# Kernel optimization log

Measured on AMD Instinct MI355X. Metric: run time of the kernel, lower is better.

## Reference

```python
import jax, jax.numpy as jnp
import numpy as np

B, G, D, L, NH = 4, 30, 320, 4, 8
DK = D // NH
S = G * G
FF = 4 * D
EPS = 1e-5

FLOAT_KEYS = ['pe', 'in_emb_w', 'in_emb_b', 'wq', 'bq', 'wk', 'bk', 'wv', 'bv', 'wo', 'bo',
              'ln_a_g', 'ln_a_b', 'dist_emb', 'dir_emb', 'w_rot', 'b_rot', 'w_refl', 'b_refl',
              'w_tr', 'b_tr', 'w_sc', 'b_sc', 'tn_w1', 'tn_b1', 'tn_w2', 'tn_b2', 'tn_w3', 'tn_b3',
              'ff_w1', 'ff_b1', 'ff_w2', 'ff_b2', 'ln2_g', 'ln2_b', 'ck1', 'cb1', 'ck3', 'cb3',
              'ck5', 'cb5', 'ck7', 'cb7', 'fus_w', 'fus_b', 'op_w1', 'op_b1', 'op_w2', 'op_b2',
              'op_w3', 'op_b3']


def _make_pe():
    # Faithful vectorization of GeometricPositionalEncoding's triple loop.
    pe = np.zeros((G, G, D), dtype=np.float32)
    i = np.arange(0, D // 2, 2)                       # 0,2,...,158
    div = 10000.0 ** (i / D)
    h = np.arange(G, dtype=np.float64)
    sh = np.sin(h[:, None] / div)[:, None, :]
    ch = np.cos(h[:, None] / div)[:, None, :]
    pe[:, :, i] = sh
    pe[:, :, i + 1] = ch
    sw = np.sin(h[:, None] / div)[None, :, :]
    cw = np.cos(h[:, None] / div)[None, :, :]
    pe[:, :, i + D // 2] = sw
    pe[:, :, i + D // 2 + 1] = cw
    hh, ww = np.meshgrid(np.arange(G), np.arange(G), indexing='ij')
    c = G // 2
    pe[:, :, -4] = np.sqrt((hh - c) ** 2 + (ww - c) ** 2) / G   # overwrites last 4 dims, as in torch
    pe[:, :, -3] = hh / G
    pe[:, :, -2] = ww / G
    pe[:, :, -1] = (hh + ww) / (2 * G)
    return pe


def _make_geo_indices():
    # Precompute _compute_geometric_bias index tables (distance bin, direction octant).
    idx = np.arange(S)
    hc, wc = idx // G, idx % G
    dh = hc[None, :] - hc[:, None]                    # h2 - h1 at [i, j]
    dw = wc[None, :] - wc[:, None]
    dist = np.minimum(np.sqrt(dh ** 2 + dw ** 2).astype(np.int32), 59)
    ang = np.arctan2(dh.astype(np.float64), dw.astype(np.float64))
    dirn = ((ang + np.pi) / (2 * np.pi / 8)).astype(np.int32) % 8
    dirn[(dh == 0) & (dw == 0)] = 0
    return dist.astype(np.int32), dirn.astype(np.int32)


def _ln(x, g, b):
    m = x.mean(-1, keepdims=True)
    v = ((x - m) ** 2).mean(-1, keepdims=True)
    return (x - m) * jax.lax.rsqrt(v + EPS) * g + b


def _gelu(x):
    return jax.nn.gelu(x, approximate=False)  # torch nn.GELU default (erf)


def _forward(p, input_grid, dist_idx, dir_idx):
    x = jax.nn.one_hot(input_grid[:, 0], 10, dtype=jnp.float32)   # [B,G,G,10]
    x = x @ p['in_emb_w'] + p['in_emb_b']                          # [B,G,G,D]
    x = x + p['pe'][None]
    scale = 1.0 / np.sqrt(DK)
    for l in range(L):
        xs = x.reshape(B, S, D)
        def heads(w, b):
            return (xs @ w + b).reshape(B, S, NH, DK).transpose(0, 2, 1, 3)
        q = heads(p['wq'][l], p['bq'][l])
        k = heads(p['wk'][l], p['bk'][l])
        v = heads(p['wv'][l], p['bv'][l])
        # geometric bias via embedding gathers: [S,S,NH] -> [NH,S,S]
        bias = p['dist_emb'][l][dist_idx] + p['dir_emb'][l][dir_idx]
        scores = jnp.einsum('bhsd,bhtd->bhst', q, k) * scale + bias.transpose(2, 0, 1)[None]
        attn = jax.nn.softmax(scores, axis=-1)
        out = jnp.einsum('bhst,bhtd->bhsd', attn, v).transpose(0, 2, 1, 3).reshape(B, S, D)
        xs = _ln(out @ p['wo'][l] + p['bo'][l] + xs, p['ln_a_g'][l], p['ln_a_b'][l])
        # geometric transformation module
        g = xs.mean(1)                                              # [B,D] global mean over H,W
        tp = jnp.concatenate([
            jax.nn.softmax(g @ p['w_rot'][l] + p['b_rot'][l], axis=-1),
            jax.nn.softmax(g @ p['w_refl'][l] + p['b_refl'][l], axis=-1),
            jnp.tanh(g @ p['w_tr'][l] + p['b_tr'][l]),
            jax.nn.softmax(g @ p['w_sc'][l] + p['b_sc'][l], axis=-1)], axis=-1)   # [B,17]
        ti = jnp.concatenate([xs, jnp.broadcast_to(tp[:, None, :], (B, S, 17))], axis=-1)
        t = _gelu(ti @ p['tn_w1'][l] + p['tn_b1'][l])
        t = _gelu(t @ p['tn_w2'][l] + p['tn_b2'][l])
        t = t @ p['tn_w3'][l] + p['tn_b3'][l]
        xs = xs + 0.3 * t
        # feed-forward with post-LN residual
        f = _gelu(xs @ p['ff_w1'][l] + p['ff_b1'][l]) @ p['ff_w2'][l] + p['ff_b2'][l]
        xs = _ln(f + xs, p['ln2_g'][l], p['ln2_b'][l])
        x = xs.reshape(B, G, G, D)
    # multiscale conv fusion (NHWC, SAME padding == torch padding=k//2 for odd k)
    dn = ('NHWC', 'HWIO', 'NHWC')
    feats = [jax.nn.relu(jax.lax.conv_general_dilated(x, p['ck%d' % kk], (1, 1), 'SAME',
                                                      dimension_numbers=dn) + p['cb%d' % kk])
             for kk in (1, 3, 5, 7)]
    fused = jnp.concatenate(feats, axis=-1) @ p['fus_w'] + p['fus_b']
    h1 = _gelu(fused @ p['op_w1'] + p['op_b1'])
    h2 = _gelu(h1 @ p['op_w2'] + p['op_b2'])
    return h2 @ p['op_w3'] + p['op_b3']                            # [B,G,G,10] logits


def setup_inputs():
    key = jax.random.key(0)
    ks = iter(jax.random.split(key, 80))
    w = lambda *s: (0.02 * jax.random.normal(next(ks), s)).astype(jnp.float32)
    z = lambda *s: jnp.zeros(s, jnp.float32)
    inp = dict(
        input_grid=jax.random.randint(next(ks), (B, 1, G, G), 0, 10, dtype=jnp.int32),
        pe=jnp.asarray(_make_pe()),
        in_emb_w=w(10, D), in_emb_b=z(D),
        wq=w(L, D, D), bq=z(L, D), wk=w(L, D, D), bk=z(L, D),
        wv=w(L, D, D), bv=z(L, D), wo=w(L, D, D), bo=z(L, D),
        ln_a_g=jnp.ones((L, D), jnp.float32), ln_a_b=z(L, D),
        dist_emb=w(L, 60, NH), dir_emb=w(L, 8, NH),
        w_rot=w(L, D, 4), b_rot=z(L, 4), w_refl=w(L, D, 8), b_refl=z(L, 8),
        w_tr=w(L, D, 2), b_tr=z(L, 2), w_sc=w(L, D, 3), b_sc=z(L, 3),
        tn_w1=w(L, D + 17, 2 * D), tn_b1=z(L, 2 * D),
        tn_w2=w(L, 2 * D, D), tn_b2=z(L, D),
        tn_w3=w(L, D, D), tn_b3=z(L, D),
        ff_w1=w(L, D, FF), ff_b1=z(L, FF), ff_w2=w(L, FF, D), ff_b2=z(L, D),
        ln2_g=jnp.ones((L, D), jnp.float32), ln2_b=z(L, D),
        ck1=w(1, 1, D, D), cb1=z(D), ck3=w(3, 3, D, D), cb3=z(D),
        ck5=w(5, 5, D, D), cb5=z(D), ck7=w(7, 7, D, D), cb7=z(D),
        fus_w=w(4 * D, D), fus_b=z(D),
        op_w1=w(D, D // 2), op_b1=z(D // 2),
        op_w2=w(D // 2, D // 4), op_b2=z(D // 4),
        op_w3=w(D // 4, 10), op_b3=z(10),
    )
    di, dr = _make_geo_indices()
    inp['dist_idx'] = jnp.asarray(di)
    inp['dir_idx'] = jnp.asarray(dr)
    return inp


def reference(input_grid, dist_idx, dir_idx, pe, in_emb_w, in_emb_b, wq, bq, wk, bk, wv, bv, wo, bo,
              ln_a_g, ln_a_b, dist_emb, dir_emb, w_rot, b_rot, w_refl, b_refl, w_tr, b_tr, w_sc, b_sc,
              tn_w1, tn_b1, tn_w2, tn_b2, tn_w3, tn_b3, ff_w1, ff_b1, ff_w2, ff_b2, ln2_g, ln2_b,
              ck1, cb1, ck3, cb3, ck5, cb5, ck7, cb7, fus_w, fus_b,
              op_w1, op_b1, op_w2, op_b2, op_w3, op_b3):
    p = dict(zip(FLOAT_KEYS, (pe, in_emb_w, in_emb_b, wq, bq, wk, bk, wv, bv, wo, bo,
                              ln_a_g, ln_a_b, dist_emb, dir_emb, w_rot, b_rot, w_refl, b_refl,
                              w_tr, b_tr, w_sc, b_sc, tn_w1, tn_b1, tn_w2, tn_b2, tn_w3, tn_b3,
                              ff_w1, ff_b1, ff_w2, ff_b2, ln2_g, ln2_b, ck1, cb1, ck3, cb3,
                              ck5, cb5, ck7, cb7, fus_w, fus_b, op_w1, op_b1, op_w2, op_b2,
                              op_w3, op_b3)))
    return _forward(p, input_grid, dist_idx, dir_idx)
```

## Files before the change

### kernel.cpp

```cpp
#include <hip/hip_runtime.h>
#include <hip/hip_bf16.h>

#define BB 4
#define GG_ 30
#define DD 320
#define LL 4
#define NHH 8
#define DKK 40
#define SS 900
#define BS 3600
#define FFD 1280
#define LDK 72

typedef __attribute__((ext_vector_type(8))) short short8;
typedef __attribute__((ext_vector_type(4))) short short4v;
typedef __attribute__((ext_vector_type(4))) float f32x4;

__device__ __forceinline__ float gelu_f(float x) {
    return 0.5f * x * (1.0f + erff(x * 0.70710678118654752f));
}

__device__ __forceinline__ float bfbits2f(short b) {
    return __uint_as_float(((unsigned)(unsigned short)b) << 16);
}

__device__ __forceinline__ void convt_tile(const float* __restrict__ s,
                                           __hip_bfloat16* __restrict__ d,
                                           int K, int N, int Kpad, int kb, int nb) {
    __shared__ float t[32][33];
    const int tx = threadIdx.x, ty = threadIdx.y;
#pragma unroll
    for (int i = 0; i < 4; ++i) {
        int k = kb + ty + i * 8, n = nb + tx;
        t[ty + i * 8][tx] = (k < K && n < N) ? s[(size_t)k * N + n] : 0.f;
    }
    __syncthreads();
#pragma unroll
    for (int i = 0; i < 4; ++i) {
        int n = nb + ty + i * 8, k = kb + tx;
        if (n < N && k < Kpad) d[(size_t)n * Kpad + k] = __float2bfloat16(t[tx][ty + i * 8]);
    }
}

__global__ __launch_bounds__(256) void allconvt_kernel(
    const float* wo, const float* tnw1, const float* tnw2, const float* tnw3,
    const float* ffw1, const float* ffw2, const float* ck1, const float* ck3,
    const float* ck5, const float* ck7, const float* fusw, const float* opw1,
    __hip_bfloat16* WOT, __hip_bfloat16* TN1T, __hip_bfloat16* TN2T, __hip_bfloat16* TN3T,
    __hip_bfloat16* FF1T, __hip_bfloat16* FF2T, __hip_bfloat16* CK1T, __hip_bfloat16* CK3T,
    __hip_bfloat16* CK5T, __hip_bfloat16* CK7T, __hip_bfloat16* FUST, __hip_bfloat16* OP1T) {
    const int bid = blockIdx.x;
    const float* s; __hip_bfloat16* d;
    int K, N, Kpad, gx, per, local, sS, dS;
    if (bid < 400)        { local = bid;         s = wo;   d = WOT;  K = 320;  N = 320;  Kpad = 320;  sS = 102400; dS = 102400; gx = 10;  per = 100; }
    else if (bid < 1360)  { local = bid - 400;   s = tnw1; d = TN1T; K = 337;  N = 640;  Kpad = 384;  sS = 215680; dS = 245760; gx = 12;  per = 240; }
    else if (bid < 2160)  { local = bid - 1360;  s = tnw2; d = TN2T; K = 640;  N = 320;  Kpad = 640;  sS = 204800; dS = 204800; gx = 20;  per = 200; }
    else if (bid < 2560)  { local = bid - 2160;  s = tnw3; d = TN3T; K = 320;  N = 320;  Kpad = 320;  sS = 102400; dS = 102400; gx = 10;  per = 100; }
    else if (bid < 4160)  { local = bid - 2560;  s = ffw1; d = FF1T; K = 320;  N = 1280; Kpad = 320;  sS = 409600; dS = 409600; gx = 10;  per = 400; }
    else if (bid < 5760)  { local = bid - 4160;  s = ffw2; d = FF2T; K = 1280; N = 320;  Kpad = 1280; sS = 409600; dS = 409600; gx = 40;  per = 400; }
    else if (bid < 5860)  { local = bid - 5760;  s = ck1;  d = CK1T; K = 320;  N = 320;  Kpad = 320;  sS = 0; dS = 0; gx = 10;  per = 100; }
    else if (bid < 6760)  { local = bid - 5860;  s = ck3;  d = CK3T; K = 2880; N = 320;  Kpad = 2880; sS = 0; dS = 0; gx = 90;  per = 900; }
    else if (bid < 9260)  { local = bid - 6760;  s = ck5;  d = CK5T; K = 8000; N = 320;  Kpad = 8000; sS = 0; dS = 0; gx = 250; per = 2500; }
    else if (bid < 14160) { local = bid - 9260;  s = ck7;  d = CK7T; K = 15680; N = 320; Kpad = 15680; sS = 0; dS = 0; gx = 490; per = 4900; }
    else if (bid < 14560) { local = bid - 14160; s = fusw; d = FUST; K = 1280; N = 320;  Kpad = 1280; sS = 0; dS = 0; gx = 40;  per = 400; }
    else                  { local = bid - 14560; s = opw1; d = OP1T; K = 320;  N = 160;  Kpad = 320;  sS = 0; dS = 0; gx = 10;  per = 50; }
    const int mat = local / per, rem = local - mat * per;
    const int kb = (rem % gx) * 32, nb = (rem / gx) * 32;
    convt_tile(s + (size_t)mat * sS, d + (size_t)mat * dS, K, N, Kpad, kb, nb);
}

__global__ __launch_bounds__(256) void qkvconvt_kernel(const float* __restrict__ wq,
                                                       const float* __restrict__ wk,
                                                       const float* __restrict__ wv,
                                                       __hip_bfloat16* __restrict__ dst) {
    __shared__ float t[32][33];
    const int z = blockIdx.z, l = z / 3, wsel = z % 3;
    const float* s = (wsel == 0 ? wq : wsel == 1 ? wk : wv) + (size_t)l * 102400;
    __hip_bfloat16* d = dst + (size_t)l * 307200 + wsel * 102400;
    const int kb = blockIdx.x * 32, nb = blockIdx.y * 32;
    const int tx = threadIdx.x, ty = threadIdx.y;
#pragma unroll
    for (int i = 0; i < 4; ++i) {
        int k = kb + ty + i * 8, n = nb + tx;
        t[ty + i * 8][tx] = s[(size_t)k * 320 + n];
    }
    __syncthreads();
#pragma unroll
    for (int i = 0; i < 4; ++i) {
        int n = nb + ty + i * 8, k = kb + tx;
        d[(size_t)n * 320 + k] = __float2bfloat16(t[tx][ty + i * 8]);
    }
}

__global__ void embed_kernel(const int* __restrict__ grid, const float* __restrict__ pe,
                             const float* __restrict__ ew, const float* __restrict__ eb,
                             float* __restrict__ x, __hip_bfloat16* __restrict__ xb) {
    int idx = blockIdx.x * 256 + threadIdx.x;
    int m = idx / DD, d = idx % DD;
    int gv = grid[m];
    float v = ew[gv * DD + d] + eb[d] + pe[(m % SS) * DD + d];
    x[idx] = v;
    xb[idx] = __float2bfloat16(v);
}

__global__ __launch_bounds__(256) void mgemm_kernel(
    const __hip_bfloat16* __restrict__ A, int lda,
    const __hip_bfloat16* __restrict__ Aaux,
    const __hip_bfloat16* __restrict__ Wt, int ldw,
    const float* __restrict__ bias, const float* __restrict__ biasB, const float* __restrict__ biasC,
    const float* __restrict__ res, int ldr,
    float alpha, float* __restrict__ Cf, float* __restrict__ Cf2,
    __hip_bfloat16* __restrict__ Cb, int ldc,
    int M, int N, int K, int act) {
    __shared__ short As[128 * LDK];
    __shared__ short Bs[64 * LDK];
    const int tid = threadIdx.x;
    const int m0 = blockIdx.y * 128, n0 = blockIdx.x * 64;
    const int kb0 = blockIdx.z * K;
    float* __restrict__ CfO = (blockIdx.z == 0) ? Cf : Cf2;
    const int lane = tid & 63;
    const int w = tid >> 6, wm = w >> 1, wn = w & 1;
    const int rbase = tid >> 3, q8 = (tid & 7) * 8;
    f32x4 acc[4][2];
    const f32x4 fz = {0.f, 0.f, 0.f, 0.f};
#pragma unroll
    for (int mi = 0; mi < 4; ++mi)
#pragma unroll
        for (int ni = 0; ni < 2; ++ni) acc[mi][ni] = fz;
    const short8 zz = {0, 0, 0, 0, 0, 0, 0, 0};
    for (int k0 = 0; k0 < K; k0 += 64) {
        const int gk = kb0 + k0;
        const bool auxChunk = (Aaux != nullptr) && (gk == 320);
#pragma unroll
        for (int c = 0; c < 4; ++c) {
            int r = c * 32 + rbase, m = m0 + r;
            short8 v = zz;
            if (m < M) {
                if (auxChunk) {
                    int bidx = m / SS;
#pragma unroll
                    for (int e = 0; e < 8; ++e) {
                        int j = q8 + e;
                        v[e] = (j < 17) ? ((const short*)Aaux)[bidx * 17 + j] : (short)0;
                    }
                } else {
                    v = *(const short8*)((const short*)A + (size_t)m * lda + gk + q8);
                }
            }
            *(short8*)(As + r * LDK + q8) = v;
        }
#pragma unroll
        for (int c = 0; c < 2; ++c) {
            int r = c * 32 + rbase, n = n0 + r;
            short8 v = zz;
            if (n < N) v = *(const short8*)((const short*)Wt + (size_t)n * ldw + gk + q8);
            *(short8*)(Bs + r * LDK + q8) = v;
        }
        __syncthreads();
#pragma unroll
        for (int ks = 0; ks < 64; ks += 32) {
            const int kb = ks + (lane >> 4) * 8;
            short8 af[4], bf[2];
#pragma unroll
            for (int mi = 0; mi < 4; ++mi)
                af[mi] = *(const short8*)(As + (wm * 64 + mi * 16 + (lane & 15)) * LDK + kb);
#pragma unroll
            for (int ni = 0; ni < 2; ++ni)
                bf[ni] = *(const short8*)(Bs + (wn * 32 + ni * 16 + (lane & 15)) * LDK + kb);
#pragma unroll
            for (int mi = 0; mi < 4; ++mi)
#pragma unroll
                for (int ni = 0; ni < 2; ++ni)
                    acc[mi][ni] = __builtin_amdgcn_mfma_f32_16x16x32_bf16(af[mi], bf[ni], acc[mi][ni], 0, 0, 0);
        }
        __syncthreads();
    }
    const int col0 = n0 + wn * 32 + (lane & 15);
    const int rloc = (lane >> 4) * 4;
#pragma unroll
    for (int mi = 0; mi < 4; ++mi) {
#pragma unroll
        for (int ni = 0; ni < 2; ++ni) {
            int col = col0 + ni * 16;
            if (col >= N) continue;
            float bv;
            if (biasC) bv = (col < 320) ? bias[col] : (col < 640) ? biasB[col - 320] : biasC[col - 640];
            else bv = bias ? bias[col] : 0.f;
#pragma unroll
            for (int r = 0; r < 4; ++r) {
                int row = m0 + wm * 64 + mi * 16 + rloc + r;
                if (row >= M) continue;
                float v = acc[mi][ni][r] + bv;
                if (act == 1) v = gelu_f(v);
                else if (act == 2) v = fmaxf(v, 0.f);
                v *= alpha;
                if (res) v += res[(size_t)row * ldr + col];
                if (CfO) CfO[(size_t)row * ldc + col] = v;
                if (Cb) Cb[(size_t)row * ldc + col] = __float2bfloat16(v);
            }
        }
    }
}

__global__ __launch_bounds__(256) void mconvall_kernel(
    const __hip_bfloat16* __restrict__ P, const __hip_bfloat16* __restrict__ W3,
    const __hip_bfloat16* __restrict__ W5, const __hip_bfloat16* __restrict__ W7,
    __hip_bfloat16* __restrict__ part) {
    const int nwg = 1160;
    const int ib = blockIdx.x;
    const int xcd = ib & 7, kk2 = ib >> 3;
    const int qq = nwg >> 3, rr = nwg & 7;
    const int wid = (xcd < rr) ? (xcd * (qq + 1) + kk2) : (rr * (qq + 1) + (xcd - rr) * qq + kk2);
    const int seg = wid / 145, local = wid - seg * 145;
    int KS, t0, t1;
    const __hip_bfloat16* Wt;
    if (seg == 0)      { KS = 3; Wt = W3; t0 = 0; t1 = 9; }
    else if (seg == 1) { KS = 5; Wt = W5; t0 = 0; t1 = 13; }
    else if (seg == 2) { KS = 5; Wt = W5; t0 = 13; t1 = 25; }
    else               { KS = 7; Wt = W7; int z = seg - 3; t0 = z * 10; t1 = (z < 4) ? t0 + 10 : 49; }
    const int slice = seg;
    const int K = KS * KS * DD;
    const int OFF = 3 - KS / 2;
    const int mt = local % 29, nt = local / 29;
    __hip_bfloat16* __restrict__ Cp = part + (size_t)slice * BS * DD;
    __shared__ short As[128 * LDK];
    __shared__ short Bs[64 * LDK];
    const int tid = threadIdx.x;
    const int m0 = mt * 128, n0 = nt * 64;
    const int lane = tid & 63;
    const int w = tid >> 6, wm = w >> 1, wn = w & 1;
    const int rbase = tid >> 3, q8 = (tid & 7) * 8;
    f32x4 acc[4][2];
    const f32x4 fz = {0.f, 0.f, 0.f, 0.f};
#pragma unroll
    for (int mi = 0; mi < 4; ++mi)
#pragma unroll
        for (int ni = 0; ni < 2; ++ni) acc[mi][ni] = fz;
    const short8 zz = {0, 0, 0, 0, 0, 0, 0, 0};
    const short* P0[4];
    bool mval[4];
#pragma unroll
    for (int c = 0; c < 4; ++c) {
        int m = m0 + c * 32 + rbase;
        mval[c] = (m < BS);
        int mm = mval[c] ? m : 0;
        int b = mm / SS, hw = mm % SS, oh = hw / GG_, ow = hw % GG_;
        P0[c] = (const short*)P + (size_t)((b * 36 + oh) * 36 + ow) * DD + q8;
    }
    const short* W0[2];
#pragma unroll
    for (int c = 0; c < 2; ++c) {
        int n = n0 + c * 32 + rbase;
        W0[c] = (const short*)Wt + (size_t)n * K + q8;
    }
    for (int tap = t0; tap < t1; ++tap) {
        const int khr = tap / KS, kw = tap - khr * KS;
        const int tapOff = ((khr + OFF) * 36 + (kw + OFF)) * DD;
        const int wOff = tap * DD;
        for (int ci0 = 0; ci0 < DD; ci0 += 64) {
#pragma unroll
            for (int c = 0; c < 4; ++c) {
                int r = c * 32 + rbase;
                short8 v = mval[c] ? *(const short8*)(P0[c] + tapOff + ci0) : zz;
                *(short8*)(As + r * LDK + q8) = v;
            }
#pragma unroll
            for (int c = 0; c < 2; ++c) {
                int r = c * 32 + rbase;
                short8 v = *(const short8*)(W0[c] + wOff + ci0);
                *(short8*)(Bs + r * LDK + q8) = v;
            }
            __syncthreads();
#pragma unroll
            for (int ks = 0; ks < 64; ks += 32) {
                const int kb = ks + (lane >> 4) * 8;
                short8 af[4], bf[2];
#pragma unroll
                for (int mi = 0; mi < 4; ++mi)
                    af[mi] = *(const short8*)(As + (wm * 64 + mi * 16 + (lane & 15)) * LDK + kb);
#pragma unroll
                for (int ni = 0; ni < 2; ++ni)
                    bf[ni] = *(const short8*)(Bs + (wn * 32 + ni * 16 + (lane & 15)) * LDK + kb);
#pragma unroll
                for (int mi = 0; mi < 4; ++mi)
#pragma unroll
                    for (int ni = 0; ni < 2; ++ni)
                        acc[mi][ni] = __builtin_amdgcn_mfma_f32_16x16x32_bf16(af[mi], bf[ni], acc[mi][ni], 0, 0, 0);
            }
            __syncthreads();
        }
    }
    const int col0 = n0 + wn * 32 + (lane & 15);
    const int rloc = (lane >> 4) * 4;
#pragma unroll
    for (int mi = 0; mi < 4; ++mi) {
#pragma unroll
        for (int ni = 0; ni < 2; ++ni) {
            int col = col0 + ni * 16;
#pragma unroll
            for (int r = 0; r < 4; ++r) {
                int row = m0 + wm * 64 + mi * 16 + rloc + r;
                if (row < BS) Cp[(size_t)row * DD + col] = __float2bfloat16(acc[mi][ni][r]);
            }
        }
    }
}

__global__ __launch_bounds__(256) void creduceall_kernel(const __hip_bfloat16* __restrict__ part,
                                                         const float* __restrict__ cb3,
                                                         const float* __restrict__ cb5,
                                                         const float* __restrict__ cb7,
                                                         __hip_bfloat16* __restrict__ feats) {
    const int PER = BS * DD / 8;
    int idx = blockIdx.x * 256 + threadIdx.x;
    int which = idx / PER;
    if (which >= 3) return;
    int sub = idx - which * PER;
    int row = sub / (DD / 8), c8 = (sub % (DD / 8)) * 8;
    const __hip_bfloat16* basep;
    const float* bias;
    int nsplit, colOff;
    if (which == 0)      { basep = part;                          nsplit = 1; bias = cb3; colOff = 320; }
    else if (which == 1) { basep = part + (size_t)1 * BS * DD;    nsplit = 2; bias = cb5; colOff = 640; }
    else                 { basep = part + (size_t)3 * BS * DD;    nsplit = 5; bias = cb7; colOff = 960; }
    float s[8] = {};
    for (int p = 0; p < nsplit; ++p) {
        short8 v = *(const short8*)((const short*)basep + (size_t)p * BS * DD + (size_t)row * DD + c8);
#pragma unroll
        for (int j = 0; j < 8; ++j) s[j] += bfbits2f(v[j]);
    }
    __hip_bfloat16* o = feats + (size_t)row * 1280 + colOff + c8;
#pragma unroll
    for (int j = 0; j < 8; ++j) o[j] = __float2bfloat16(fmaxf(s[j] + bias[c8 + j], 0.f));
}

__global__ void pad_kernel(const __hip_bfloat16* __restrict__ xb, __hip_bfloat16* __restrict__ p) {
    int idx = blockIdx.x * 256 + threadIdx.x;
    if (idx >= BB * 36 * 36 * DD) return;
    int c = idx % DD, t = idx / DD;
    int wp = t % 36, t2 = t / 36, hp = t2 % 36, b = t2 / 36;
    __hip_bfloat16 v = __float2bfloat16(0.f);
    if (hp >= 3 && hp < 33 && wp >= 3 && wp < 33)
        v = xb[((b * SS + (hp - 3) * GG_ + (wp - 3))) * DD + c];
    p[idx] = v;
}

__global__ __launch_bounds__(256) void gemm_kernel(
    const float* __restrict__ A, int lda, const float* __restrict__ W,
    const float* __restrict__ bias, float* __restrict__ C, int ldc,
    int M, int N, int K, int act) {
    __shared__ float As[16][65];
    __shared__ float Ws[16][65];
    const int tid = threadIdx.x;
    const int m0 = blockIdx.y * 64, n0 = blockIdx.x * 64;
    const int tx = tid & 15, ty = tid >> 4;
    float acc[4][4] = {};
    const int kkA = tid & 15, mloc0 = tid >> 4;
    const int nloc = tid & 63, kk0 = tid >> 6;
    for (int k0 = 0; k0 < K; k0 += 16) {
        const int kA = k0 + kkA;
#pragma unroll
        for (int i = 0; i < 4; ++i) {
            int mloc = mloc0 + i * 16, m = m0 + mloc;
            As[kkA][mloc] = (m < M && kA < K) ? A[m * lda + kA] : 0.f;
        }
#pragma unroll
        for (int i = 0; i < 4; ++i) {
            int kk = kk0 + i * 4, k = k0 + kk, n = n0 + nloc;
            Ws[kk][nloc] = (k < K && n < N) ? W[k * N + n] : 0.f;
        }
        __syncthreads();
#pragma unroll
        for (int kk = 0; kk < 16; ++kk) {
            float a[4], b[4];
#pragma unroll
            for (int i = 0; i < 4; ++i) a[i] = As[kk][ty * 4 + i];
#pragma unroll
            for (int j = 0; j < 4; ++j) b[j] = Ws[kk][tx * 4 + j];
#pragma unroll
            for (int i = 0; i < 4; ++i)
#pragma unroll
                for (int j = 0; j < 4; ++j) acc[i][j] = fmaf(a[i], b[j], acc[i][j]);
        }
        __syncthreads();
    }
#pragma unroll
    for (int i = 0; i < 4; ++i) {
        int m = m0 + ty * 4 + i;
        if (m >= M) continue;
#pragma unroll
        for (int j = 0; j < 4; ++j) {
            int n = n0 + tx * 4 + j;
            if (n >= N) continue;
            float v = acc[i][j] + bias[n];
            if (act == 1) v = gelu_f(v);
            C[m * ldc + n] = v;
        }
    }
}

__global__ __launch_bounds__(256) void attprep_kernel(const float* __restrict__ de,
                                                      const float* __restrict__ dre,
                                                      const int* __restrict__ dist,
                                                      const int* __restrict__ dirn,
                                                      const __hip_bfloat16* __restrict__ QKV,
                                                      __hip_bfloat16* __restrict__ biasOut,
                                                      __hip_bfloat16* __restrict__ VT) {
    const int gid = blockIdx.x;
    const int tid = threadIdx.x;
    if (gid < 3375) {
        int idx = gid * 256 + tid;
        int sq = idx / 960, t = idx - sq * 960;
        float lut[NHH];
        if (t < SS) {
            int dv = dist[sq * SS + t], rv = dirn[sq * SS + t];
#pragma unroll
            for (int h = 0; h < NHH; ++h) lut[h] = de[dv * NHH + h] + dre[rv * NHH + h];
        } else {
#pragma unroll
            for (int h = 0; h < NHH; ++h) lut[h] = 0.f;
        }
#pragma unroll
        for (int h = 0; h < NHH; ++h)
            biasOut[((size_t)h * SS + sq) * 960 + t] = __float2bfloat16(lut[h]);
    } else {
        int vidx = (gid - 3375) * 256 + tid;
        int t0 = (vidx % 240) * 4;
        int d = (vidx / 240) % 48;
        int h = (vidx / (240 * 48)) % NHH;
        int b = vidx / (240 * 48 * NHH);
        short4v v = {0, 0, 0, 0};
        if (d < DKK) {
#pragma unroll
            for (int j = 0; j < 4; ++j) {
                int t = t0 + j;
                if (t < SS)
                    v[j] = ((const short*)QKV)[((size_t)b * SS + t) * 960 + 640 + h * DKK + d];
            }
        }
        *(short4v*)((short*)VT + (((size_t)b * NHH + h) * 48 + d) * 960 + t0) = v;
    }
}

#define LQ 72
#define LK 72
#define LV 72
#define LP 72
__global__ __launch_bounds__(512) void mattn_kernel(
    const __hip_bfloat16* __restrict__ Qg, const __hip_bfloat16* __restrict__ Kg,
    const __hip_bfloat16* __restrict__ VTg, const __hip_bfloat16* __restrict__ BIASg,
    __hip_bfloat16* __restrict__ AO) {
    const int qt = blockIdx.x, h = blockIdx.y, b = blockIdx.z;
    const int tid = threadIdx.x, lane = tid & 63, w = tid >> 6;
    const int wq = w & 3, ws = w >> 2;
    const int tid2 = tid & 255;
    const int lhi = lane >> 4, llo = lane & 15;
    __shared__ short Qs[64 * LQ];
    __shared__ short Ks[2][64 * LK];
    __shared__ short Vs[2][48 * LV];
    __shared__ short Ps[8][16 * LP];
    __shared__ float Lm[4][16];
    __shared__ float Ll[4][16];
    __shared__ float Lo[4][16][DKK];
    short* Ps_w = Ps[w];
    short* Ks_s = Ks[ws];
    short* Vs_s = Vs[ws];
    const int q0 = qt * 64;
    const short4v z4 = {0, 0, 0, 0};
    const f32x4 fz = {0.f, 0.f, 0.f, 0.f};
    const float scale = 0.15811388300841898f;

    for (int task = tid; task < 64 * 16; task += 512) {
        int r = task >> 4, d0 = (task & 15) * 4;
        int q = q0 + r;
        short4v v = z4;
        if (q < SS && d0 < DKK)
            v = *(const short4v*)((const short*)Qg + ((size_t)b * SS + q) * 960 + h * DKK + d0);
        *(short4v*)(Qs + r * LQ + d0) = v;
    }
    __syncthreads();
    short8 qa[2];
#pragma unroll
    for (int ks = 0; ks < 2; ++ks)
        qa[ks] = *(const short8*)(Qs + (wq * 16 + llo) * LQ + ks * 32 + lhi * 8);

    float mrow[4] = {-1e30f, -1e30f, -1e30f, -1e30f};
    float lrow[4] = {0.f, 0.f, 0.f, 0.f};
    f32x4 o[3] = {fz, fz, fz};
    const int qrow = q0 + wq * 16 + lhi * 4;

    for (int tt = 0; tt < 8; ++tt) {
        const int t = tt * 2 + ws;
        const int kv0 = t * 64;
        if (t < 15) {
            for (int task = tid2; task < 64 * 16; task += 256) {
                int r = task >> 4, d0 = (task & 15) * 4;
                int kv = kv0 + r;
                short4v v = z4;
                if (kv < SS && d0 < DKK)
                    v = *(const short4v*)((const short*)Kg + ((size_t)b * SS + kv) * 960 + h * DKK + d0);
                *(short4v*)(Ks_s + r * LK + d0) = v;
            }
            for (int task = tid2; task < 48 * 16; task += 256) {
                int r = task >> 4, c4 = (task & 15) * 4;
                short4v v = *(const short4v*)((const short*)VTg +
                             (((size_t)b * NHH + h) * 48 + r) * 960 + kv0 + c4);
                *(short4v*)(Vs_s + r * LV + c4) = v;
            }
        }
        __syncthreads();
        if (t < 15) {
            f32x4 s[4] = {fz, fz, fz, fz};
#pragma unroll
            for (int ks = 0; ks < 2; ++ks) {
#pragma unroll
                for (int ni = 0; ni < 4; ++ni) {
                    short8 kb = *(const short8*)(Ks_s + (ni * 16 + llo) * LK + ks * 32 + lhi * 8);
                    s[ni] = __builtin_amdgcn_mfma_f32_16x16x32_bf16(qa[ks], kb, s[ni], 0, 0, 0);
                }
            }
#pragma unroll
            for (int ni = 0; ni < 4; ++ni) {
                int col = kv0 + ni * 16 + llo;
#pragma unroll
                for (int r = 0; r < 4; ++r) {
                    int qc = qrow + r; if (qc > SS - 1) qc = SS - 1;
                    float v = s[ni][r] * scale +
                              __bfloat162float(BIASg[((size_t)h * SS + qc) * 960 + col]);
                    s[ni][r] = (col < SS) ? v : -1e30f;
                }
            }
            float rmax[4], psum[4], corr[4];
#pragma unroll
            for (int r = 0; r < 4; ++r)
                rmax[r] = fmaxf(fmaxf(s[0][r], s[1][r]), fmaxf(s[2][r], s[3][r]));
#pragma unroll
            for (int off = 1; off < 16; off <<= 1)
#pragma unroll
                for (int r = 0; r < 4; ++r)
                    rmax[r] = fmaxf(rmax[r], __shfl_xor(rmax[r], off));
#pragma unroll
            for (int r = 0; r < 4; ++r) {
                float mnew = fmaxf(mrow[r], rmax[r]);
                corr[r] = __expf(mrow[r] - mnew);
                mrow[r] = mnew;
                float ps = 0.f;
#pragma unroll
                for (int ni = 0; ni < 4; ++ni) {
                    float p = __expf(s[ni][r] - mnew);
                    s[ni][r] = p;
                    ps += p;
                }
                psum[r] = ps;
            }
#pragma unroll
            for (int off = 1; off < 16; off <<= 1)
#pragma unroll
                for (int r = 0; r < 4; ++r) psum[r] += __shfl_xor(psum[r], off);
#pragma unroll
            for (int r = 0; r < 4; ++r) lrow[r] = lrow[r] * corr[r] + psum[r];
#pragma unroll
            for (int nj = 0; nj < 3; ++nj)
#pragma unroll
                for (int r = 0; r < 4; ++r) o[nj][r] *= corr[r];
#pragma unroll
            for (int ni = 0; ni < 4; ++ni)
#pragma unroll
                for (int r = 0; r < 4; ++r)
                    ((__hip_bfloat16*)Ps_w)[(lhi * 4 + r) * LP + ni * 16 + llo] =
                        __float2bfloat16(s[ni][r]);
#pragma unroll
            for (int ks = 0; ks < 2; ++ks) {
                short8 pa = *(const short8*)(Ps_w + llo * LP + ks * 32 + lhi * 8);
#pragma unroll
                for (int nj = 0; nj < 3; ++nj) {
                    short8 vb = *(const short8*)(Vs_s + (nj * 16 + llo) * LV + ks * 32 + lhi * 8);
                    o[nj] = __builtin_amdgcn_mfma_f32_16x16x32_bf16(pa, vb, o[nj], 0, 0, 0);
                }
            }
        }
        __syncthreads();
    }
    if (ws == 1) {
#pragma unroll
        for (int r = 0; r < 4; ++r) {
            int lr = lhi * 4 + r;
            if (llo == 0) { Lm[wq][lr] = mrow[r]; Ll[wq][lr] = lrow[r]; }
#pragma unroll
            for (int nj = 0; nj < 3; ++nj) {
                int d = nj * 16 + llo;
                if (d < DKK) Lo[wq][lr][d] = o[nj][r];
            }
        }
    }
    __syncthreads();
    if (ws == 0) {
#pragma unroll
        for (int r = 0; r < 4; ++r) {
            int lr = lhi * 4 + r;
            float m1 = Lm[wq][lr], l1 = Ll[wq][lr];
            float m = fmaxf(mrow[r], m1);
            float a0 = __expf(mrow[r] - m), a1 = __expf(m1 - m);
            float linv = 1.f / (lrow[r] * a0 + l1 * a1);
            int q = qrow + r;
            if (q < SS) {
#pragma unroll
                for (int nj = 0; nj < 3; ++nj) {
                    int d = nj * 16 + llo;
                    if (d < DKK)
                        AO[((size_t)b * SS + q) * DD + h * DKK + d] =
                            __float2bfloat16((o[nj][r] * a0 + Lo[wq][lr][d] * a1) * linv);
                }
            }
        }
    }
}

__global__ __launch_bounds__(320) void ln_kernel(const float* __restrict__ a,
                                                 const float* __restrict__ a2,
                                                 const float* __restrict__ cb,
                                                 const float* __restrict__ add,
                                                 const float* __restrict__ g,
                                                 const float* __restrict__ bta,
                                                 float* __restrict__ out,
                                                 __hip_bfloat16* __restrict__ outb) {
    const int row = blockIdx.x, i = threadIdx.x;
    __shared__ float red[320];
    __shared__ float s_m, s_v;
    float v = a[row * DD + i];
    if (a2) v += a2[row * DD + i];
    if (cb) v += cb[i];
    if (add) v += add[row * DD + i];
    red[i] = v;
    __syncthreads();
    if (i < 64) red[i] += red[i + 256];
    __syncthreads();
    for (int s = 128; s > 0; s >>= 1) {
        if (i < s) red[i] += red[i + s];
        __syncthreads();
    }
    if (i == 0) s_m = red[0] * (1.0f / DD);
    __syncthreads();
    const float d = v - s_m;
    red[i] = d * d;
    __syncthreads();
    if (i < 64) red[i] += red[i + 256];
    __syncthreads();
    for (int s = 128; s > 0; s >>= 1) {
        if (i < s) red[i] += red[i + s];
        __syncthreads();
    }
    if (i == 0) s_v = red[0] * (1.0f / DD);
    __syncthreads();
    float o = d * rsqrtf(s_v + 1e-5f) * g[i] + bta[i];
    out[row * DD + i] = o;
    outb[row * DD + i] = __float2bfloat16(o);
}

__global__ __launch_bounds__(256) void mpart_kernel(const float* __restrict__ xs,
                                                    float* __restrict__ mp) {
    const int b = blockIdx.y, z = blockIdx.z;
    const int d = blockIdx.x * 64 + (threadIdx.x & 63);
    const int rg = threadIdx.x >> 6;
    float s = 0.f;
    const int t0 = z * 150;
    for (int t = t0 + rg; t < t0 + 150; t += 4) s += xs[((size_t)b * SS + t) * DD + d];
    __shared__ float red[256];
    red[threadIdx.x] = s;
    __syncthreads();
    if (threadIdx.x < 128) red[threadIdx.x] += red[threadIdx.x + 128];
    __syncthreads();
    if (threadIdx.x < 64) mp[((size_t)b * 6 + z) * DD + d] = red[threadIdx.x] + red[threadIdx.x + 64];
}

__global__ __launch_bounds__(64) void tp_kernel(const float* __restrict__ mp,
                                                const float* __restrict__ wrot, const float* __restrict__ brot,
                                                const float* __restrict__ wrefl, const float* __restrict__ brefl,
                                                const float* __restrict__ wtr, const float* __restrict__ btr,
                                                const float* __restrict__ wsc, const float* __restrict__ bsc,
                                                __hip_bfloat16* __restrict__ tpb) {
    const int b = blockIdx.x, tid = threadIdx.x;
    __shared__ float gs[DD];
    __shared__ float raw[17];
    for (int j = tid; j < DD; j += 64) {
        float s6 = 0.f;
#pragma unroll
        for (int z = 0; z < 6; ++z) s6 += mp[((size_t)b * 6 + z) * DD + j];
        gs[j] = s6 * (1.0f / SS);
    }
    __syncthreads();
    if (tid < 17) {
        float s;
        if (tid < 4) {
            s = brot[tid];
            for (int d = 0; d < DD; ++d) s = fmaf(gs[d], wrot[d * 4 + tid], s);
        } else if (tid < 12) {
            int j = tid - 4;
            s = brefl[j];
            for (int d = 0; d < DD; ++d) s = fmaf(gs[d], wrefl[d * 8 + j], s);
        } else if (tid < 14) {
            int j = tid - 12;
            s = btr[j];
            for (int d = 0; d < DD; ++d) s = fmaf(gs[d], wtr[d * 2 + j], s);
        } else {
            int j = tid - 14;
            s = bsc[j];
            for (int d = 0; d < DD; ++d) s = fmaf(gs[d], wsc[d * 3 + j], s);
        }
        raw[tid] = s;
    }
    __syncthreads();
    if (tid == 0) {
        float mx = -1e30f;
        for (int j = 0; j < 4; ++j) mx = fmaxf(mx, raw[j]);
        float sm = 0.f, e[4];
        for (int j = 0; j < 4; ++j) { e[j] = expf(raw[j] - mx); sm += e[j]; }
        for (int j = 0; j < 4; ++j) tpb[b * 17 + j] = __float2bfloat16(e[j] / sm);
    } else if (tid == 1) {
        float mx = -1e30f;
        for (int j = 4; j < 12; ++j) mx = fmaxf(mx, raw[j]);
        float sm = 0.f, e[8];
        for (int j = 0; j < 8; ++j) { e[j] = expf(raw[4 + j] - mx); sm += e[j]; }
        for (int j = 0; j < 8; ++j) tpb[b * 17 + 4 + j] = __float2bfloat16(e[j] / sm);
    } else if (tid == 2) {
        tpb[b * 17 + 12] = __float2bfloat16(tanhf(raw[12]));
        tpb[b * 17 + 13] = __float2bfloat16(tanhf(raw[13]));
    } else if (tid == 3) {
        float mx = -1e30f;
        for (int j = 14; j < 17; ++j) mx = fmaxf(mx, raw[j]);
        float sm = 0.f, e[3];
        for (int j = 0; j < 3; ++j) { e[j] = expf(raw[14 + j] - mx); sm += e[j]; }
        for (int j = 0; j < 3; ++j) tpb[b * 17 + 14 + j] = __float2bfloat16(e[j] / sm);
    }
}

static inline void launch_mgemm(hipStream_t s, const __hip_bfloat16* A, int lda,
                                const __hip_bfloat16* Aaux,
                                const __hip_bfloat16* Wt, int ldw, const float* bias,
                                const float* biasB, const float* biasC,
                                const float* res, int ldr, float alpha, float* Cf,
                                __hip_bfloat16* Cb, int ldc, int M, int N, int K, int act) {
    dim3 g((N + 63) / 64, (M + 127) / 128);
    mgemm_kernel<<<g, 256, 0, s>>>(A, lda, Aaux, Wt, ldw, bias, biasB, biasC, res, ldr, alpha,
                                   Cf, nullptr, Cb, ldc, M, N, K, act);
}

extern "C" void kernel_launch(void* const* d_in, const int* in_sizes, int n_in,
                              void* d_out, int out_size, void* d_ws, size_t ws_size,
                              hipStream_t stream) {
    (void)in_sizes; (void)n_in; (void)out_size; (void)ws_size;
    const int* in_grid = (const int*)d_in[0];
    const float* pe = (const float*)d_in[1];
    const float* iew = (const float*)d_in[2];
    const float* ieb = (const float*)d_in[3];
    const float* wq = (const float*)d_in[4], *bq = (const float*)d_in[5];
    const float* wk = (const float*)d_in[6], *bk = (const float*)d_in[7];
    const float* wv = (const float*)d_in[8], *bv = (const float*)d_in[9];
    const float* wo = (const float*)d_in[10], *bo = (const float*)d_in[11];
    const float* lnag = (const float*)d_in[12], *lnab = (const float*)d_in[13];
    const float* dist_emb = (const float*)d_in[14], *dir_emb = (const float*)d_in[15];
    const float* wrot = (const float*)d_in[16], *brot = (const float*)d_in[17];
    const float* wrefl = (const float*)d_in[18], *brefl = (const float*)d_in[19];
    const float* wtr = (const float*)d_in[20], *btr = (const float*)d_in[21];
    const float* wsc = (const float*)d_in[22], *bsc = (const float*)d_in[23];
    const float* tnw1 = (const float*)d_in[24], *tnb1 = (const float*)d_in[25];
    const float* tnw2 = (const float*)d_in[26], *tnb2 = (const float*)d_in[27];
    const float* tnw3 = (const float*)d_in[28], *tnb3 = (const float*)d_in[29];
    const float* ffw1 = (const float*)d_in[30], *ffb1 = (const float*)d_in[31];
    const float* ffw2 = (const float*)d_in[32], *ffb2 = (const float*)d_in[33];
    const float* ln2g = (const float*)d_in[34], *ln2b = (const float*)d_in[35];
    const float* ck1 = (const float*)d_in[36], *cb1 = (const float*)d_in[37];
    const float* ck3 = (const float*)d_in[38], *cb3 = (const float*)d_in[39];
    const float* ck5 = (const float*)d_in[40], *cb5 = (const float*)d_in[41];
    const float* ck7 = (const float*)d_in[42], *cb7 = (const float*)d_in[43];
    const float* fusw = (const float*)d_in[44], *fusb = (const float*)d_in[45];
    const float* opw1 = (const float*)d_in[46], *opb1 = (const float*)d_in[47];
    const float* opw2 = (const float*)d_in[48], *opb2 = (const float*)d_in[49];
    const float* opw3 = (const float*)d_in[50], *opb3 = (const float*)d_in[51];
    const int* dist_idx = (const int*)d_in[52];
    const int* dir_idx = (const int*)d_in[53];
    float* out = (float*)d_out;

    char* base = (char*)d_ws;
    typedef __hip_bfloat16 bf;
    bf* WQKVT = (bf*)(base + 0);
    bf* WOT = (bf*)(base + 2457600);
    bf* TN1T = (bf*)(base + 3276800);
    bf* TN2T = (bf*)(base + 5242880);
    bf* TN3T = (bf*)(base + 6881280);
    bf* FF1T = (bf*)(base + 7700480);
    bf* FF2T = (bf*)(base + 10977280);
    bf* CK1T = (bf*)(base + 14254080);
    bf* CK3T = (bf*)(base + 14458880);
    bf* CK5T = (bf*)(base + 16302080);
    bf* CK7T = (bf*)(base + 21422080);
    bf* FUST = (bf*)(base + 31457280);
    bf* OP1T = (bf*)(base + 32276480);
    float* XS = (float*)(base + 32378880);
    bf* XSbf = (bf*)(base + 36986880);
    bf* QKVbf = (bf*)(base + 39290880);
    bf* VT = (bf*)(base + 46202880);
    float* P1f = (float*)(base + 39290880);
    float* R2 = (float*)(base + 53114880);
    bf* TPbf = (bf*)(base + 57728000);
    bf* CPART = (bf*)(base + 39290880);
    char* BIG = base + 57728512;
    bf* AObf = (bf*)(BIG + 0);
    float* MPart = (float*)(BIG + 0);
    bf* BIAS = (bf*)(BIG + 2764800);
    bf* T1bf = (bf*)(BIG + 2764800);
    bf* T2bf = (bf*)(BIG + 7372800);
    bf* F1bf = (bf*)(BIG + 0);
    bf* PADbf = (bf*)(BIG + 0);
    bf* FEATSbf = (bf*)(BIG + 3317760);
    float* H1 = (float*)(BIG + 0);
    float* H2 = (float*)(BIG + 2304000);
    bf* R2bf = XSbf;

    dim3 cb(32, 8);
    qkvconvt_kernel<<<dim3(10, 10, 12), cb, 0, stream>>>(wq, wk, wv, WQKVT);
    allconvt_kernel<<<14610, cb, 0, stream>>>(wo, tnw1, tnw2, tnw3, ffw1, ffw2,
                                              ck1, ck3, ck5, ck7, fusw, opw1,
                                              WOT, TN1T, TN2T, TN3T, FF1T, FF2T,
                                              CK1T, CK3T, CK5T, CK7T, FUST, OP1T);

    embed_kernel<<<4500, 256, 0, stream>>>(in_grid, pe, iew, ieb, XS, XSbf);

    for (int l = 0; l < LL; ++l) {
        const int wO = l * DD * DD, bO = l * DD;
        launch_mgemm(stream, XSbf, DD, nullptr, WQKVT + l * 307200, 320, bq + bO, bk + bO, bv + bO,
                     nullptr, 0, 1.f, nullptr, QKVbf, 960, BS, 960, 320, 0);
        attprep_kernel<<<4815, 256, 0, stream>>>(dist_emb + l * 60 * NHH, dir_emb + l * 8 * NHH,
                                                 dist_idx, dir_idx, QKVbf, BIAS, VT);
        mattn_kernel<<<dim3(15, NHH, BB), 512, 0, stream>>>(QKVbf, QKVbf + 320, VT, BIAS, AObf);
        launch_mgemm(stream, AObf, DD, nullptr, WOT + wO, DD, bo + bO, nullptr, nullptr, XS, DD, 1.f,
                     R2, nullptr, DD, BS, DD, DD, 0);
        ln_kernel<<<BS, 320, 0, stream>>>(R2, nullptr, nullptr, nullptr, lnag + bO, lnab + bO, XS, XSbf);
        mpart_kernel<<<dim3(5, BB, 6), 256, 0, stream>>>(XS, MPart);
        tp_kernel<<<BB, 64, 0, stream>>>(MPart, wrot + l * 1280, brot + l * 4,
                                         wrefl + l * 2560, brefl + l * 8,
                                         wtr + l * 640, btr + l * 2,
                                         wsc + l * 960, bsc + l * 3, TPbf);
        launch_mgemm(stream, XSbf, DD, TPbf, TN1T + l * 245760, 384, tnb1 + l * 640, nullptr,
                     nullptr, nullptr, 0, 1.f, nullptr, T1bf, 640, BS, 640, 384, 1);
        launch_mgemm(stream, T1bf, 640, nullptr, TN2T + l * 204800, 640, tnb2 + bO, nullptr,
                     nullptr, nullptr, 0, 1.f, nullptr, T2bf, DD, BS, DD, 640, 1);
        launch_mgemm(stream, T2bf, DD, nullptr, TN3T + wO, DD, tnb3 + bO, nullptr, nullptr, XS, DD,
                     0.3f, XS, XSbf, DD, BS, DD, DD, 0);
        launch_mgemm(stream, XSbf, DD, nullptr, FF1T + l * 409600, DD, ffb1 + l * FFD, nullptr,
                     nullptr, nullptr, 0, 1.f, nullptr, F1bf, FFD, BS, FFD, DD, 1);
        {
            dim3 g(5, 29, 2);
            mgemm_kernel<<<g, 256, 0, stream>>>(F1bf, FFD, nullptr, FF2T + l * 409600, FFD,
                                                nullptr, nullptr, nullptr, nullptr, 0, 1.f,
                                                R2, P1f, nullptr, DD, BS, DD, 640, 0);
        }
        ln_kernel<<<BS, 320, 0, stream>>>(R2, P1f, ffb2 + bO, XS, ln2g + bO, ln2b + bO, XS, XSbf);
    }

    pad_kernel<<<(BB * 36 * 36 * DD + 255) / 256, 256, 0, stream>>>(XSbf, PADbf);
    launch_mgemm(stream, XSbf, DD, nullptr, CK1T, DD, cb1, nullptr, nullptr, nullptr, 0, 1.f,
                 nullptr, FEATSbf + 0, 1280, BS, DD, DD, 2);
    mconvall_kernel<<<1160, 256, 0, stream>>>(PADbf, CK3T, CK5T, CK7T, CPART);
    creduceall_kernel<<<(3 * BS * DD / 8 + 255) / 256, 256, 0, stream>>>(CPART, cb3, cb5, cb7, FEATSbf);
    launch_mgemm(stream, FEATSbf, 1280, nullptr, FUST, 1280, fusb, nullptr, nullptr, nullptr, 0, 1.f,
                 nullptr, R2bf, DD, BS, DD, 1280, 0);
    launch_mgemm(stream, R2bf, DD, nullptr, OP1T, DD, opb1, nullptr, nullptr, nullptr, 0, 1.f,
                 H1, nullptr, 160, BS, 160, DD, 1);
    gemm_kernel<<<dim3(2, 57), 256, 0, stream>>>(H1, 160, opw2, opb2, H2, 80, BS, 80, 160, 1);
    gemm_kernel<<<dim3(1, 57), 256, 0, stream>>>(H2, 80, opw3, opb3, out, 10, BS, 10, 80, 0);
}
```

Baseline: 1.556 ms.

## Load Q/K/V MFMA fragments directly from global memory, drop shared staging and barriers

The attention kernel no longer stages Q, K and V tiles in shared memory. Each wave loads its MFMA operand fragments straight from global memory (clamping rows and zero-filling the padded head dimension), which removes the per-tile __syncthreads barriers and lets the two wave groups run independently. In exchange, every wave re-reads the K/V fragments from global memory or L2 instead of sharing one tile among four waves, and the loads are less coalesced.

```diff
diff --git a/kernel.cpp b/kernel.cpp
--- a/kernel.cpp
+++ b/kernel.cpp
@@ -442,9 +442,6 @@
     }
 }
 
-#define LQ 72
-#define LK 72
-#define LV 72
 #define LP 72
 __global__ __launch_bounds__(512) void mattn_kernel(
     const __hip_bfloat16* __restrict__ Qg, const __hip_bfloat16* __restrict__ Kg,
@@ -453,133 +450,104 @@
     const int qt = blockIdx.x, h = blockIdx.y, b = blockIdx.z;
     const int tid = threadIdx.x, lane = tid & 63, w = tid >> 6;
     const int wq = w & 3, ws = w >> 2;
-    const int tid2 = tid & 255;
     const int lhi = lane >> 4, llo = lane & 15;
-    __shared__ short Qs[64 * LQ];
-    __shared__ short Ks[2][64 * LK];
-    __shared__ short Vs[2][48 * LV];
     __shared__ short Ps[8][16 * LP];
     __shared__ float Lm[4][16];
     __shared__ float Ll[4][16];
     __shared__ float Lo[4][16][DKK];
     short* Ps_w = Ps[w];
-    short* Ks_s = Ks[ws];
-    short* Vs_s = Vs[ws];
     const int q0 = qt * 64;
-    const short4v z4 = {0, 0, 0, 0};
+    const short8 zz = {0, 0, 0, 0, 0, 0, 0, 0};
     const f32x4 fz = {0.f, 0.f, 0.f, 0.f};
     const float scale = 0.15811388300841898f;
 
-    for (int task = tid; task < 64 * 16; task += 512) {
-        int r = task >> 4, d0 = (task & 15) * 4;
-        int q = q0 + r;
-        short4v v = z4;
-        if (q < SS && d0 < DKK)
-            v = *(const short4v*)((const short*)Qg + ((size_t)b * SS + q) * 960 + h * DKK + d0);
-        *(short4v*)(Qs + r * LQ + d0) = v;
-    }
-    __syncthreads();
     short8 qa[2];
-#pragma unroll
-    for (int ks = 0; ks < 2; ++ks)
-        qa[ks] = *(const short8*)(Qs + (wq * 16 + llo) * LQ + ks * 32 + lhi * 8);
+    {
+        int qr = q0 + wq * 16 + llo;
+        if (qr > SS - 1) qr = SS - 1;
+        const short* qp = (const short*)Qg + ((size_t)b * SS + qr) * 960 + h * DKK;
+        qa[0] = *(const short8*)(qp + lhi * 8);
+        qa[1] = (lhi == 0) ? *(const short8*)(qp + 32) : zz;
+    }
 
     float mrow[4] = {-1e30f, -1e30f, -1e30f, -1e30f};
     float lrow[4] = {0.f, 0.f, 0.f, 0.f};
     f32x4 o[3] = {fz, fz, fz};
     const int qrow = q0 + wq * 16 + lhi * 4;
-
-    for (int tt = 0; tt < 8; ++tt) {
-        const int t = tt * 2 + ws;
+    const short* Vbase = (const short*)VTg + (((size_t)b * NHH + h) * 48) * 960;
+
+    for (int t = ws; t < 15; t += 2) {
         const int kv0 = t * 64;
-        if (t < 15) {
-            for (int task = tid2; task < 64 * 16; task += 256) {
-                int r = task >> 4, d0 = (task & 15) * 4;
-                int kv = kv0 + r;
-                short4v v = z4;
-                if (kv < SS && d0 < DKK)
-                    v = *(const short4v*)((const short*)Kg + ((size_t)b * SS + kv) * 960 + h * DKK + d0);
-                *(short4v*)(Ks_s + r * LK + d0) = v;
-            }
-            for (int task = tid2; task < 48 * 16; task += 256) {
-                int r = task >> 4, c4 = (task & 15) * 4;
-                short4v v = *(const short4v*)((const short*)VTg +
-                             (((size_t)b * NHH + h) * 48 + r) * 960 + kv0 + c4);
-                *(short4v*)(Vs_s + r * LV + c4) = v;
-            }
-        }
-        __syncthreads();
-        if (t < 15) {
-            f32x4 s[4] = {fz, fz, fz, fz};
-#pragma unroll
-            for (int ks = 0; ks < 2; ++ks) {
-#pragma unroll
-                for (int ni = 0; ni < 4; ++ni) {
-                    short8 kb = *(const short8*)(Ks_s + (ni * 16 + llo) * LK + ks * 32 + lhi * 8);
-                    s[ni] = __builtin_amdgcn_mfma_f32_16x16x32_bf16(qa[ks], kb, s[ni], 0, 0, 0);
-                }
-            }
+        f32x4 s[4] = {fz, fz, fz, fz};
+#pragma unroll
+        for (int ni = 0; ni < 4; ++ni) {
+            int kr = kv0 + ni * 16 + llo;
+            if (kr > SS - 1) kr = SS - 1;
+            const short* kp = (const short*)Kg + ((size_t)b * SS + kr) * 960 + h * DKK;
+            short8 kb0 = *(const short8*)(kp + lhi * 8);
+            short8 kb1 = (lhi == 0) ? *(const short8*)(kp + 32) : zz;
+            s[ni] = __builtin_amdgcn_mfma_f32_16x16x32_bf16(qa[0], kb0, s[ni], 0, 0, 0);
+            s[ni] = __builtin_amdgcn_mfma_f32_16x16x32_bf16(qa[1], kb1, s[ni], 0, 0, 0);
+        }
+#pragma unroll
+        for (int ni = 0; ni < 4; ++ni) {
+            int col = kv0 + ni * 16 + llo;
+#pragma unroll
+            for (int r = 0; r < 4; ++r) {
+                int qc = qrow + r; if (qc > SS - 1) qc = SS - 1;
+                float v = s[ni][r] * scale +
+                          __bfloat162float(BIASg[((size_t)h * SS + qc) * 960 + col]);
+                s[ni][r] = (col < SS) ? v : -1e30f;
+            }
+        }
+        float rmax[4], psum[4], corr[4];
+#pragma unroll
+        for (int r = 0; r < 4; ++r)
+            rmax[r] = fmaxf(fmaxf(s[0][r], s[1][r]), fmaxf(s[2][r], s[3][r]));
+#pragma unroll
+        for (int off = 1; off < 16; off <<= 1)
+#pragma unroll
+            for (int r = 0; r < 4; ++r)
+                rmax[r] = fmaxf(rmax[r], __shfl_xor(rmax[r], off));
+#pragma unroll
+        for (int r = 0; r < 4; ++r) {
+            float mnew = fmaxf(mrow[r], rmax[r]);
+            corr[r] = __expf(mrow[r] - mnew);
+            mrow[r] = mnew;
+            float ps = 0.f;
 #pragma unroll
             for (int ni = 0; ni < 4; ++ni) {
-                int col = kv0 + ni * 16 + llo;
-#pragma unroll
-                for (int r = 0; r < 4; ++r) {
-                    int qc = qrow + r; if (qc > SS - 1) qc = SS - 1;
-                    float v = s[ni][r] * scale +
-                              __bfloat162float(BIASg[((size_t)h * SS + qc) * 960 + col]);
-                    s[ni][r] = (col < SS) ? v : -1e30f;
-                }
-            }
-            float rmax[4], psum[4], corr[4];
+                float p = __expf(s[ni][r] - mnew);
+                s[ni][r] = p;
+                ps += p;
+            }
+            psum[r] = ps;
+        }
+#pragma unroll
+        for (int off = 1; off < 16; off <<= 1)
+#pragma unroll
+            for (int r = 0; r < 4; ++r) psum[r] += __shfl_xor(psum[r], off);
+#pragma unroll
+        for (int r = 0; r < 4; ++r) lrow[r] = lrow[r] * corr[r] + psum[r];
+#pragma unroll
+        for (int nj = 0; nj < 3; ++nj)
+#pragma unroll
+            for (int r = 0; r < 4; ++r) o[nj][r] *= corr[r];
+#pragma unroll
+        for (int ni = 0; ni < 4; ++ni)
 #pragma unroll
             for (int r = 0; r < 4; ++r)
-                rmax[r] = fmaxf(fmaxf(s[0][r], s[1][r]), fmaxf(s[2][r], s[3][r]));
-#pragma unroll
-            for (int off = 1; off < 16; off <<= 1)
-#pragma unroll
-                for (int r = 0; r < 4; ++r)
-                    rmax[r] = fmaxf(rmax[r], __shfl_xor(rmax[r], off));
-#pragma unroll
-            for (int r = 0; r < 4; ++r) {
-                float mnew = fmaxf(mrow[r], rmax[r]);
-                corr[r] = __expf(mrow[r] - mnew);
-                mrow[r] = mnew;
-                float ps = 0.f;
-#pragma unroll
-                for (int ni = 0; ni < 4; ++ni) {
-                    float p = __expf(s[ni][r] - mnew);
-                    s[ni][r] = p;
-                    ps += p;
-                }
-                psum[r] = ps;
-            }
-#pragma unroll
-            for (int off = 1; off < 16; off <<= 1)
-#pragma unroll
-                for (int r = 0; r < 4; ++r) psum[r] += __shfl_xor(psum[r], off);
-#pragma unroll
-            for (int r = 0; r < 4; ++r) lrow[r] = lrow[r] * corr[r] + psum[r];
-#pragma unroll
-            for (int nj = 0; nj < 3; ++nj)
-#pragma unroll
-                for (int r = 0; r < 4; ++r) o[nj][r] *= corr[r];
-#pragma unroll
-            for (int ni = 0; ni < 4; ++ni)
-#pragma unroll
-                for (int r = 0; r < 4; ++r)
-                    ((__hip_bfloat16*)Ps_w)[(lhi * 4 + r) * LP + ni * 16 + llo] =
-                        __float2bfloat16(s[ni][r]);
-#pragma unroll
-            for (int ks = 0; ks < 2; ++ks) {
-                short8 pa = *(const short8*)(Ps_w + llo * LP + ks * 32 + lhi * 8);
-#pragma unroll
-                for (int nj = 0; nj < 3; ++nj) {
-                    short8 vb = *(const short8*)(Vs_s + (nj * 16 + llo) * LV + ks * 32 + lhi * 8);
-                    o[nj] = __builtin_amdgcn_mfma_f32_16x16x32_bf16(pa, vb, o[nj], 0, 0, 0);
-                }
-            }
-        }
-        __syncthreads();
+                ((__hip_bfloat16*)Ps_w)[(lhi * 4 + r) * LP + ni * 16 + llo] =
+                    __float2bfloat16(s[ni][r]);
+#pragma unroll
+        for (int ks = 0; ks < 2; ++ks) {
+            short8 pa = *(const short8*)(Ps_w + llo * LP + ks * 32 + lhi * 8);
+#pragma unroll
+            for (int nj = 0; nj < 3; ++nj) {
+                short8 vb = *(const short8*)(Vbase + (size_t)(nj * 16 + llo) * 960 + kv0 + ks * 32 + lhi * 8);
+                o[nj] = __builtin_amdgcn_mfma_f32_16x16x32_bf16(pa, vb, o[nj], 0, 0, 0);
+            }
+        }
     }
     if (ws == 1) {
 #pragma unroll
```

After: 1.579 ms. About the same (+1.5%).
